# Kernel tuning notes

Hardware: AMD Instinct MI355X
Metric: run time of the kernel (lower is better)

Reference implementation:

```python
import jax, jax.numpy as jnp
import numpy as np

K = 5   # attention window size
G = 8   # groups


def _gconv(x, w):
    # grouped 1x1 conv: x (B,H,W,G,Cin_g), w (G, Cout_g, Cin_g) -> (B,H,W,G,Cout_g)
    return jnp.einsum('bhwgi,goi->bhwgo', x, w)


def _windows(t, k):
    # t: (B, H+2p, W+2p, G, Cg) padded map -> (B, H, W, G, Cg, k*k) local windows
    p = k // 2
    H = t.shape[1] - 2 * p
    W = t.shape[2] - 2 * p
    pats = [t[:, di:di + H, dj:dj + W] for di in range(k) for dj in range(k)]
    return jnp.stack(pats, axis=-1)


def setup_inputs() -> dict:
    key = jax.random.key(0)
    ks = jax.random.split(key, 6)
    B, H, W, C, OC = 4, 56, 56, 256, 256
    Cg_in, Cg = C // G, OC // G
    x = jax.random.normal(ks[0], (B, H, W, C), jnp.float32)
    scale = 0.1  # ~kaiming-ish magnitude for 1x1 convs
    wq = jax.random.normal(ks[1], (G, Cg, Cg_in), jnp.float32) * scale
    wk = jax.random.normal(ks[2], (G, Cg, Cg_in), jnp.float32) * scale
    wv = jax.random.normal(ks[3], (G, Cg, Cg_in), jnp.float32) * scale
    rel_emb = jax.random.normal(ks[4], (G, Cg, K, K), jnp.float32)
    q_emb = jax.random.normal(ks[5], (OC,), jnp.float32)
    return {"x": x, "wq": wq, "wk": wk, "wv": wv, "rel_emb": rel_emb, "q_emb": q_emb}


def reference(x, wq, wk, wv, rel_emb, q_emb):
    B, H, W, C = x.shape
    g, Cg, _ = wq.shape
    p = K // 2
    xg = x.reshape(B, H, W, g, C // g)
    # 1x1 grouped conv projections (pad-then-conv == conv-then-pad for 1x1, no bias)
    q = _gconv(xg, wq) + q_emb.reshape(g, Cg)            # (B,H,W,G,Cg)
    k = _gconv(xg, wk)
    v = _gconv(xg, wv)
    pad = ((0, 0), (p, p), (p, p), (0, 0), (0, 0))
    kwin = _windows(jnp.pad(k, pad), K)                   # (B,H,W,G,Cg,K*K)
    vwin = _windows(jnp.pad(v, pad), K)
    kwin = kwin + rel_emb.reshape(g, Cg, K * K)           # relative position bias
    logits = q[..., None] * kwin                          # scalar q per (b,h,w,g,c)
    wts = jax.nn.softmax(logits, axis=-1)                 # per-channel softmax over K*K
    out = jnp.sum(wts * vwin, axis=-1)                    # (B,H,W,G,Cg)
    return out.reshape(B, H, W, g * Cg)
```

## Files before the change

kernel.cpp:

```cpp
#include <hip/hip_runtime.h>


constexpr int TB = 4, TH = 56, TW = 56, TC = 256;
constexpr int G  = 8, CG = 32, PAD = 2;
constexpr int TILE = 8;
constexpr int HT = TILE + 2 * PAD;
constexpr int NT = TH / TILE;
constexpr int NPIX_HALO = HT * HT;
constexpr int XP = 40;
constexpr int KP = 33;
constexpr float LOG2E = 1.44269504088896340736f;

typedef __fp16 half2_t __attribute__((ext_vector_type(2)));
typedef __fp16 half8   __attribute__((ext_vector_type(8)));
typedef float  f32x4   __attribute__((ext_vector_type(4)));

__device__ __forceinline__ unsigned h2u(half2_t h) {
    union { half2_t h; unsigned u; } cv; cv.h = h; return cv.u;
}
__device__ __forceinline__ unsigned packbf(float k, float v) {
    return ((__float_as_uint(k) + 0x8000u) >> 16) |
           ((__float_as_uint(v) + 0x8000u) & 0xffff0000u);
}

__global__ __launch_bounds__(256, 2)
void fused_attn_conv_kernel(const float* __restrict__ x,
                            const float* __restrict__ wq,
                            const float* __restrict__ wk,
                            const float* __restrict__ wv,
                            const float* __restrict__ rel,
                            const float* __restrict__ qemb,
                            float* __restrict__ out) {
    __shared__ __align__(16) __fp16 xs16[NPIX_HALO][XP];
    __shared__ __align__(16) __fp16 wTs[3 * CG][XP];
    __shared__ unsigned kvs[NPIX_HALO][KP];
    __shared__ float    qs[TILE * TILE][KP];

    const int bid  = blockIdx.x;
    const int g    = bid & 7;
    const int tile = bid >> 3;
    const int tj   = tile % NT;
    const int ti   = (tile / NT) % NT;
    const int b    = tile / (NT * NT);

    const int t  = threadIdx.x;
    const int c  = t & 31;
    const int p0 = t >> 5;

    const int oc = g * CG + c;
    const int h0 = ti * TILE - PAD, w0 = tj * TILE - PAD;

    unsigned (*xsu)[XP / 2] = (unsigned(*)[XP / 2])xs16;
#pragma unroll
    for (int r = 0; r < 9; ++r) {
        const int f  = t + r * 256;
        const int px = f >> 4, pr = f & 15;
        const int hi = px / HT, hj = px % HT;
        const int gh = h0 + hi, gw = w0 + hj;
        unsigned val = 0u;
        if (gh >= 0 && gh < TH && gw >= 0 && gw < TW) {
            const float2 xv = *(const float2*)(x + (((size_t)b * TH + gh) * TW + gw) * TC
                                                 + g * CG + pr * 2);
            val = h2u(__builtin_amdgcn_cvt_pkrtz(xv.x, xv.y));
        }
        xsu[px][pr] = val;
    }

    {
        unsigned (*wTu)[XP / 2] = (unsigned(*)[XP / 2])wTs;
        const float* wsrc[3] = {wq, wk, wv};
#pragma unroll
        for (int m = 0; m < 3; ++m) {
#pragma unroll
            for (int r = 0; r < 2; ++r) {
                const int f = t + r * 256;
                const int row = f >> 4, pr = f & 15;
                const float2 wv2 = *(const float2*)(wsrc[m] + ((size_t)(g * CG + row)) * CG
                                                            + pr * 2);
                wTu[m * CG + row][pr] = h2u(__builtin_amdgcn_cvt_pkrtz(wv2.x, wv2.y));
            }
        }
    }

    __syncthreads();

    const int wvid = t >> 6, lw = t & 63;
    const int lcol = lw & 15;
    const int lko  = (lw >> 4) * 8;
    const f32x4 z4 = {0.f, 0.f, 0.f, 0.f};

    {
        const half8 bk0 = *(const half8*)&wTs[32 + lcol][lko];
        const half8 bk1 = *(const half8*)&wTs[48 + lcol][lko];
        const half8 bv0 = *(const half8*)&wTs[64 + lcol][lko];
        const half8 bv1 = *(const half8*)&wTs[80 + lcol][lko];
#pragma unroll 1
        for (int mt = wvid; mt < 9; mt += 4) {
            const half8 a = *(const half8*)&xs16[mt * 16 + lcol][lko];
            const f32x4 dk0 = __builtin_amdgcn_mfma_f32_16x16x32_f16(a, bk0, z4, 0, 0, 0);
            const f32x4 dk1 = __builtin_amdgcn_mfma_f32_16x16x32_f16(a, bk1, z4, 0, 0, 0);
            const f32x4 dv0 = __builtin_amdgcn_mfma_f32_16x16x32_f16(a, bv0, z4, 0, 0, 0);
            const f32x4 dv1 = __builtin_amdgcn_mfma_f32_16x16x32_f16(a, bv1, z4, 0, 0, 0);
            const int prow = mt * 16 + ((lw >> 4) << 2);
#pragma unroll
            for (int j = 0; j < 4; ++j) {
                const int px = prow + j;
                kvs[px][lcol]      = packbf(dk0[j], dv0[j]);
                kvs[px][lcol + 16] = packbf(dk1[j], dv1[j]);
            }
        }
    }

    {
        const half8 bq0 = *(const half8*)&wTs[ 0 + lcol][lko];
        const half8 bq1 = *(const half8*)&wTs[16 + lcol][lko];
        const float qeL = qemb[g * CG + lcol];
        const float qeH = qemb[g * CG + lcol + 16];
#pragma unroll 1
        for (int mt = wvid; mt < 9; mt += 4) {
            const half8 a = *(const half8*)&xs16[mt * 16 + lcol][lko];
            const f32x4 dq0 = __builtin_amdgcn_mfma_f32_16x16x32_f16(a, bq0, z4, 0, 0, 0);
            const f32x4 dq1 = __builtin_amdgcn_mfma_f32_16x16x32_f16(a, bq1, z4, 0, 0, 0);
            const int prow = mt * 16 + ((lw >> 4) << 2);
#pragma unroll
            for (int j = 0; j < 4; ++j) {
                const int px = prow + j;
                const int hi2 = px / HT, hj2 = px % HT;
                if (hi2 >= PAD && hi2 < PAD + TILE && hj2 >= PAD && hj2 < PAD + TILE) {
                    const int qp = (hi2 - PAD) * TILE + (hj2 - PAD);
                    qs[qp][lcol]      = (dq0[j] + qeL) * LOG2E;
                    qs[qp][lcol + 16] = (dq1[j] + qeH) * LOG2E;
                }
            }
        }
    }

    unsigned relp[13];
    {
        const float* rp = rel + (size_t)oc * 25;
#pragma unroll
        for (int i = 0; i < 12; ++i) {
            const unsigned lo = __float_as_uint(rp[2 * i])     + 0x8000u;
            const unsigned hi = __float_as_uint(rp[2 * i + 1]) + 0x8000u;
            relp[i] = (lo >> 16) | (hi & 0xffff0000u);
        }
        relp[12] = (__float_as_uint(rp[24]) + 0x8000u) >> 16;
    }

    __syncthreads();

    float qreg[8];
#pragma unroll
    for (int ii = 0; ii < 8; ++ii) qreg[ii] = qs[ii * TILE + p0][c];

    float s_[8], a_[8];
#pragma unroll
    for (int ii = 0; ii < 8; ++ii) { s_[ii] = 0.f; a_[ii] = 0.f; }

#pragma unroll
    for (int h = 0; h < HT; ++h) {
        float kr[5], vr[5];
#pragma unroll
        for (int j = 0; j < 5; ++j) {
            const unsigned u = kvs[h * HT + p0 + j][c];
            kr[j] = __uint_as_float(u << 16);
            vr[j] = __uint_as_float(u & 0xffff0000u);
        }
#pragma unroll
        for (int ii = 0; ii < 8; ++ii) {
            const int di = h - ii;
            if (di >= 0 && di < 5) {
                const float qv = qreg[ii];
#pragma unroll
                for (int j = 0; j < 5; ++j) {
                    const int idx = di * 5 + j;
                    const unsigned ru = relp[idx >> 1];
                    const float rl = __uint_as_float((idx & 1) ? (ru & 0xffff0000u)
                                                               : (ru << 16));
                    const float e = __builtin_amdgcn_exp2f(qv * (kr[j] + rl));
                    s_[ii] += e;
                    a_[ii] = fmaf(e, vr[j], a_[ii]);
                }
            }
        }
    }

#pragma unroll
    for (int ii = 0; ii < 8; ++ii) {
        const int gh = ti * TILE + ii, gw = tj * TILE + p0;
        out[(((size_t)b * TH + gh) * TW + gw) * TC + g * CG + c] =
            a_[ii] * __builtin_amdgcn_rcpf(s_[ii]);
    }
}

extern "C" void kernel_launch(void* const* d_in, const int* in_sizes, int n_in,
                              void* d_out, int out_size, void* d_ws, size_t ws_size,
                              hipStream_t stream) {
    const float* x    = (const float*)d_in[0];
    const float* wq   = (const float*)d_in[1];
    const float* wk   = (const float*)d_in[2];
    const float* wv   = (const float*)d_in[3];
    const float* rel  = (const float*)d_in[4];
    const float* qemb = (const float*)d_in[5];
    float* out = (float*)d_out;

    const int nblocks = TB * NT * NT * G;
    hipLaunchKernelGGL(fused_attn_conv_kernel, dim3(nblocks), dim3(256), 0, stream,
                       x, wq, wk, wv, rel, qemb, out);
}
```

Baseline: 40.20 us.

## Load weight fragments directly to registers and fuse Q/K/V projection loops

Drops the shared-memory staging of the three weight matrices and has each lane load its MFMA B fragments straight from global memory, converting them to fp16 in registers. The separate Q projection loop is merged into the K/V loop so each x tile fragment is read from LDS once for all six MFMAs. The kv/q LDS row pitch changes from 33 to 34 and the x staging loop is only partially unrolled. This cuts LDS footprint and a pass over shared memory, at the cost of more global loads per lane and higher register pressure in the fused loop.

```diff
diff --git a/kernel.cpp b/kernel.cpp
--- a/kernel.cpp
+++ b/kernel.cpp
@@ -8,7 +8,7 @@
 constexpr int NT = TH / TILE;
 constexpr int NPIX_HALO = HT * HT;
 constexpr int XP = 40;
-constexpr int KP = 33;
+constexpr int KP = 34;
 constexpr float LOG2E = 1.44269504088896340736f;
 
 typedef __fp16 half2_t __attribute__((ext_vector_type(2)));
@@ -22,6 +22,19 @@
     return ((__float_as_uint(k) + 0x8000u) >> 16) |
            ((__float_as_uint(v) + 0x8000u) & 0xffff0000u);
 }
+__device__ __forceinline__ half8 load_w_frag(const float* __restrict__ w,
+                                             int row, int ko) {
+    const float4 a = *(const float4*)(w + (size_t)row * CG + ko);
+    const float4 b = *(const float4*)(w + (size_t)row * CG + ko + 4);
+    const half2_t h0 = __builtin_amdgcn_cvt_pkrtz(a.x, a.y);
+    const half2_t h1 = __builtin_amdgcn_cvt_pkrtz(a.z, a.w);
+    const half2_t h2 = __builtin_amdgcn_cvt_pkrtz(b.x, b.y);
+    const half2_t h3 = __builtin_amdgcn_cvt_pkrtz(b.z, b.w);
+    half8 h;
+    h[0]=h0[0]; h[1]=h0[1]; h[2]=h1[0]; h[3]=h1[1];
+    h[4]=h2[0]; h[5]=h2[1]; h[6]=h3[0]; h[7]=h3[1];
+    return h;
+}
 
 __global__ __launch_bounds__(256, 2)
 void fused_attn_conv_kernel(const float* __restrict__ x,
@@ -32,7 +45,6 @@
                             const float* __restrict__ qemb,
                             float* __restrict__ out) {
     __shared__ __align__(16) __fp16 xs16[NPIX_HALO][XP];
-    __shared__ __align__(16) __fp16 wTs[3 * CG][XP];
     __shared__ unsigned kvs[NPIX_HALO][KP];
     __shared__ float    qs[TILE * TILE][KP];
 
@@ -51,7 +63,7 @@
     const int h0 = ti * TILE - PAD, w0 = tj * TILE - PAD;
 
     unsigned (*xsu)[XP / 2] = (unsigned(*)[XP / 2])xs16;
-#pragma unroll
+#pragma unroll 3
     for (int r = 0; r < 9; ++r) {
         const int f  = t + r * 256;
         const int px = f >> 4, pr = f & 15;
@@ -66,37 +78,27 @@
         xsu[px][pr] = val;
     }
 
-    {
-        unsigned (*wTu)[XP / 2] = (unsigned(*)[XP / 2])wTs;
-        const float* wsrc[3] = {wq, wk, wv};
-#pragma unroll
-        for (int m = 0; m < 3; ++m) {
-#pragma unroll
-            for (int r = 0; r < 2; ++r) {
-                const int f = t + r * 256;
-                const int row = f >> 4, pr = f & 15;
-                const float2 wv2 = *(const float2*)(wsrc[m] + ((size_t)(g * CG + row)) * CG
-                                                            + pr * 2);
-                wTu[m * CG + row][pr] = h2u(__builtin_amdgcn_cvt_pkrtz(wv2.x, wv2.y));
-            }
-        }
-    }
-
     __syncthreads();
 
-    const int wvid = t >> 6, lw = t & 63;
-    const int lcol = lw & 15;
-    const int lko  = (lw >> 4) * 8;
-    const f32x4 z4 = {0.f, 0.f, 0.f, 0.f};
+    {
+        const int wvid = t >> 6, lw = t & 63;
+        const int lcol = lw & 15;
+        const int lko  = (lw >> 4) * 8;
+        const half8 bq0 = load_w_frag(wq, g * CG + lcol,      lko);
+        const half8 bq1 = load_w_frag(wq, g * CG + lcol + 16, lko);
+        const half8 bk0 = load_w_frag(wk, g * CG + lcol,      lko);
+        const half8 bk1 = load_w_frag(wk, g * CG + lcol + 16, lko);
+        const half8 bv0 = load_w_frag(wv, g * CG + lcol,      lko);
+        const half8 bv1 = load_w_frag(wv, g * CG + lcol + 16, lko);
+        const float qeL = qemb[g * CG + lcol];
+        const float qeH = qemb[g * CG + lcol + 16];
+        const f32x4 z4 = {0.f, 0.f, 0.f, 0.f};
 
-    {
-        const half8 bk0 = *(const half8*)&wTs[32 + lcol][lko];
-        const half8 bk1 = *(const half8*)&wTs[48 + lcol][lko];
-        const half8 bv0 = *(const half8*)&wTs[64 + lcol][lko];
-        const half8 bv1 = *(const half8*)&wTs[80 + lcol][lko];
 #pragma unroll 1
         for (int mt = wvid; mt < 9; mt += 4) {
             const half8 a = *(const half8*)&xs16[mt * 16 + lcol][lko];
+            const f32x4 dq0 = __builtin_amdgcn_mfma_f32_16x16x32_f16(a, bq0, z4, 0, 0, 0);
+            const f32x4 dq1 = __builtin_amdgcn_mfma_f32_16x16x32_f16(a, bq1, z4, 0, 0, 0);
             const f32x4 dk0 = __builtin_amdgcn_mfma_f32_16x16x32_f16(a, bk0, z4, 0, 0, 0);
             const f32x4 dk1 = __builtin_amdgcn_mfma_f32_16x16x32_f16(a, bk1, z4, 0, 0, 0);
             const f32x4 dv0 = __builtin_amdgcn_mfma_f32_16x16x32_f16(a, bv0, z4, 0, 0, 0);
@@ -107,24 +109,6 @@
                 const int px = prow + j;
                 kvs[px][lcol]      = packbf(dk0[j], dv0[j]);
                 kvs[px][lcol + 16] = packbf(dk1[j], dv1[j]);
-            }
-        }
-    }
-
-    {
-        const half8 bq0 = *(const half8*)&wTs[ 0 + lcol][lko];
-        const half8 bq1 = *(const half8*)&wTs[16 + lcol][lko];
-        const float qeL = qemb[g * CG + lcol];
-        const float qeH = qemb[g * CG + lcol + 16];
-#pragma unroll 1
-        for (int mt = wvid; mt < 9; mt += 4) {
-            const half8 a = *(const half8*)&xs16[mt * 16 + lcol][lko];
-            const f32x4 dq0 = __builtin_amdgcn_mfma_f32_16x16x32_f16(a, bq0, z4, 0, 0, 0);
-            const f32x4 dq1 = __builtin_amdgcn_mfma_f32_16x16x32_f16(a, bq1, z4, 0, 0, 0);
-            const int prow = mt * 16 + ((lw >> 4) << 2);
-#pragma unroll
-            for (int j = 0; j < 4; ++j) {
-                const int px = prow + j;
                 const int hi2 = px / HT, hj2 = px % HT;
                 if (hi2 >= PAD && hi2 < PAD + TILE && hj2 >= PAD && hj2 < PAD + TILE) {
                     const int qp = (hi2 - PAD) * TILE + (hj2 - PAD);
```

Result: slower. 43.57 us (+8.4%).
